# Kernel tuning notes

Hardware: AMD Instinct MI355X
Metric: run time of the kernel (lower is better)

Reference implementation:

```python
import jax, jax.numpy as jnp
import numpy as np

PH, PW = 7, 7
SPATIAL_SCALE = 1.0


def setup_inputs() -> dict:
    key = jax.random.key(0)
    kf, kb, kx, ky = jax.random.split(key, 4)
    B, C, H, W, R = 4, 256, 50, 50, 300
    feature_maps = jax.random.normal(kf, (B, C, H, W), dtype=jnp.float32)
    bidx = jax.random.randint(kb, (R,), 0, B).astype(jnp.float32)
    xs = jax.random.uniform(kx, (R, 2), minval=0.0, maxval=W - 1.0)
    ys = jax.random.uniform(ky, (R, 2), minval=0.0, maxval=H - 1.0)
    x_min = jnp.min(xs, axis=1)
    x_max = jnp.max(xs, axis=1)
    y_min = jnp.min(ys, axis=1)
    y_max = jnp.max(ys, axis=1)
    rois = jnp.stack([x_min, y_min, x_max, y_max, bidx], axis=1)  # [R,5]
    return {"feature_maps": feature_maps, "rois": rois}


def _roi_pool(feature_maps, rois):
    B, C, H, W = feature_maps.shape
    s = SPATIAL_SCALE
    r = rois * s                              # first scale application (as in source)
    batch_idx = r[:, 4].astype(jnp.int32)     # int() truncation of scaled batch index
    # second scale application + round + clamp, faithful to source's double-scaling
    x0 = jnp.clip(jnp.round(r[:, 0] * s), 0, W - 1).astype(jnp.int32)
    x1 = jnp.clip(jnp.round(r[:, 2] * s), 0, W - 1).astype(jnp.int32)
    y0 = jnp.clip(jnp.round(r[:, 1] * s), 0, H - 1).astype(jnp.int32)
    y1 = jnp.clip(jnp.round(r[:, 3] * s), 0, H - 1).astype(jnp.int32)
    x1 = jnp.maximum(x1, x0 + 1)
    y1 = jnp.maximum(y1, y0 + 1)
    roi_w = x1 - x0                           # >= 1, so every adaptive bin is nonempty
    roi_h = y1 - y0

    Kw = -(-W // PW)                          # max adaptive bin width  (ceil(W/PW))
    Kh = -(-H // PH)                          # max adaptive bin height (ceil(H/PH))

    # adaptive_max_pool2d bin edges: start = floor(i*size/out), end = ceil((i+1)*size/out)
    pw = jnp.arange(PW)
    wstart = x0[:, None] + (pw[None, :] * roi_w[:, None]) // PW                       # [R,PW]
    wend = x0[:, None] + ((pw[None, :] + 1) * roi_w[:, None] + PW - 1) // PW          # [R,PW]
    kw = jnp.arange(Kw)
    wpos = wstart[:, :, None] + kw[None, None, :]                                      # [R,PW,Kw]
    widx = jnp.clip(wpos, 0, W - 1)
    wvalid = wpos < wend[:, :, None]

    ph = jnp.arange(PH)
    hstart = y0[:, None] + (ph[None, :] * roi_h[:, None]) // PH
    hend = y0[:, None] + ((ph[None, :] + 1) * roi_h[:, None] + PH - 1) // PH
    kh = jnp.arange(Kh)
    hpos = hstart[:, :, None] + kh[None, None, :]                                      # [R,PH,Kh]
    hidx = jnp.clip(hpos, 0, H - 1)
    hvalid = hpos < hend[:, :, None]

    NEG = jnp.finfo(feature_maps.dtype).min
    fm = feature_maps[batch_idx]              # [R,C,H,W] per-ROI source map

    def gather_w(fm_r, widx_r):               # fm_r [C,H,W], widx_r [PW,Kw]
        return fm_r[:, :, widx_r]             # [C,H,PW,Kw]

    g = jax.vmap(gather_w)(fm, widx)          # [R,C,H,PW,Kw]
    A = jnp.max(jnp.where(wvalid[:, None, None, :, :], g, NEG), axis=-1)  # [R,C,H,PW]

    def gather_h(A_r, hidx_r):                # A_r [C,H,PW], hidx_r [PH,Kh]
        return A_r[:, hidx_r, :]              # [C,PH,Kh,PW]

    g2 = jax.vmap(gather_h)(A, hidx)          # [R,C,PH,Kh,PW]
    out = jnp.max(jnp.where(hvalid[:, None, :, :, None], g2, NEG), axis=3)  # [R,C,PH,PW]
    return out


def reference(feature_maps, rois):
    return _roi_pool(feature_maps, rois)
```

## Files before the change

kernel.cpp:

```cpp
#include <hip/hip_runtime.h>
#include <hip/hip_bf16.h>
#include <float.h>

#define B_  4
#define C_  256
#define H_  50
#define W_  50
#define R_  300
#define PH_ 7
#define PW_ 7
#define S_  (H_ * W_)
#define Q_  (PH_ * PW_)
#define SC_ (S_ * C_)
#define CQ_  64
#define NCQ  (C_ / CQ_)
#define NWG_POOL (R_ * NCQ)

__global__ __launch_bounds__(256) void transpose_tables(
    const float* __restrict__ fm,
    float* __restrict__ fmT,
    float* __restrict__ P2,
    float* __restrict__ P4)
{
    __shared__ float tile[64][69];

    const int b  = blockIdx.z;
    const int c0 = blockIdx.y * 64;
    const int s0 = blockIdx.x * 64;

    const int tx = threadIdx.x;
    const int ty = threadIdx.y;

    if (s0 + tx < S_) {
        #pragma unroll
        for (int j = 0; j < 16; ++j) {
            const int c = c0 + ty + j * 4;
            tile[ty + j * 4][tx] = fm[((size_t)b * C_ + c) * S_ + (s0 + tx)];
        }
    }
    if (tx < 4 && s0 + 64 + tx < S_) {
        #pragma unroll
        for (int j = 0; j < 16; ++j) {
            const int c = c0 + ty + j * 4;
            tile[ty + j * 4][64 + tx] = fm[((size_t)b * C_ + c) * S_ + (s0 + 64 + tx)];
        }
    }
    __syncthreads();

    #pragma unroll
    for (int j = 0; j < 16; ++j) {
        const int s = s0 + ty + j * 4;
        if (s < S_) {
            const int ls  = ty + j * 4;
            const int w   = s % W_;
            const int rem = W_ - 1 - w;
            const float v0 = tile[tx][ls];
            float p2 = (rem >= 1) ? fmaxf(v0, tile[tx][ls + 1]) : v0;
            float p4 = p2;
            if (rem >= 2) p4 = fmaxf(p4, tile[tx][ls + 2]);
            if (rem >= 3) p4 = fmaxf(p4, tile[tx][ls + 3]);

            const size_t o = ((size_t)b * S_ + s) * C_ + (c0 + tx);
            fmT[o] = v0;
            P2[o]  = p2;
            P4[o]  = p4;
        }
    }
}

__device__ __forceinline__ void roi_decode(const float* __restrict__ rois, int r,
                                           int& b, int& x0, int& y0,
                                           int& roi_w, int& roi_h)
{
    const float* rp = rois + r * 5;
    b = (int)rp[4];
    x0      = (int)rintf(rp[0]);
    y0      = (int)rintf(rp[1]);
    int x1  = (int)rintf(rp[2]);
    int y1  = (int)rintf(rp[3]);
    x0 = min(max(x0, 0), W_ - 1);
    x1 = min(max(x1, 0), W_ - 1);
    y0 = min(max(y0, 0), H_ - 1);
    y1 = min(max(y1, 0), H_ - 1);
    x1 = max(x1, x0 + 1);
    y1 = max(y1, y0 + 1);
    roi_w = x1 - x0;
    roi_h = y1 - y0;
}

template<int WH>
__device__ __forceinline__ void pool_bins(
    const float* __restrict__ fmT, const float* __restrict__ P2,
    const float* __restrict__ P4, float* __restrict__ buf,
    int wv, int lane, int imgC,
    int x0, int y0, int roi_w, int roi_h)
{
    const int start = wv * 12 + (wv ? 1 : 0);
    const int qlast = wv * 12 + 12;

    #pragma unroll 2
    for (int k = 0; k < 13; ++k) {
        int q = start + k;
        q = (q > qlast) ? qlast : q;
        const int ph = q / PW_;
        const int pw = q - ph * PW_;
        const int ws = x0 + (pw * roi_w) / PW_;
        const int we = x0 + ((pw + 1) * roi_w + PW_ - 1) / PW_;
        const int hs = y0 + (ph * roi_h) / PH_;
        const int he = y0 + ((ph + 1) * roi_h + PH_ - 1) / PH_;
        const int ww = we - ws;

        const int sp = (ww >= 4) ? 4 : ((ww >= 2) ? 2 : 1);
        const float* tb = (ww >= 4) ? P4 : ((ww >= 2) ? P2 : fmT);
        const int colB = we - sp;

        float va[WH], vb[WH];
        #pragma unroll
        for (int kh = 0; kh < WH; ++kh) {
            int row = hs + kh;
            row = (row > he - 1) ? (he - 1) : row;
            const int ro = imgC + row * (W_ * C_);
            va[kh] = tb[ro + ws * C_];
            vb[kh] = tb[ro + colB * C_];
        }
        float m = -FLT_MAX;
        #pragma unroll
        for (int kh = 0; kh < WH; ++kh)
            m = fmaxf(m, fmaxf(va[kh], vb[kh]));

        buf[q * 65 + lane] = m;
    }
}

__global__ __launch_bounds__(256) void roi_pool_tables(
    const float* __restrict__ fmT,
    const float* __restrict__ P2,
    const float* __restrict__ P4,
    const float* __restrict__ rois,
    float* __restrict__ out)
{
    __shared__ float buf[Q_ * 65];

    const int bid = blockIdx.x;
    const int swz = (bid & 7) * (NWG_POOL / 8) + (bid >> 3);
    const int r   = swz >> 2;
    const int c0  = (swz & (NCQ - 1)) * CQ_;

    const int t    = threadIdx.x;
    const int wv   = t >> 6;
    const int lane = t & 63;

    int b, x0, y0, roi_w, roi_h;
    roi_decode(rois, r, b, x0, y0, roi_w, roi_h);

    int whmax = 1;
    #pragma unroll
    for (int i = 0; i < PH_; ++i) {
        const int hs = (i * roi_h) / PH_;
        const int he = ((i + 1) * roi_h + PH_ - 1) / PH_;
        whmax = max(whmax, he - hs);
    }

    const int imgC = b * SC_ + c0 + lane;

    switch (whmax) {
        case 1: pool_bins<1>(fmT, P2, P4, buf, wv, lane, imgC, x0, y0, roi_w, roi_h); break;
        case 2: pool_bins<2>(fmT, P2, P4, buf, wv, lane, imgC, x0, y0, roi_w, roi_h); break;
        case 3: pool_bins<3>(fmT, P2, P4, buf, wv, lane, imgC, x0, y0, roi_w, roi_h); break;
        case 4: pool_bins<4>(fmT, P2, P4, buf, wv, lane, imgC, x0, y0, roi_w, roi_h); break;
        case 5: pool_bins<5>(fmT, P2, P4, buf, wv, lane, imgC, x0, y0, roi_w, roi_h); break;
        case 6: pool_bins<6>(fmT, P2, P4, buf, wv, lane, imgC, x0, y0, roi_w, roi_h); break;
        case 7: pool_bins<7>(fmT, P2, P4, buf, wv, lane, imgC, x0, y0, roi_w, roi_h); break;
        default: pool_bins<8>(fmT, P2, P4, buf, wv, lane, imgC, x0, y0, roi_w, roi_h); break;
    }
    __syncthreads();

    float* outp = out + ((size_t)r * C_ + c0) * Q_;
    #pragma unroll
    for (int k = 0; k < 13; ++k) {
        const int e = k * 256 + t;
        if (e < CQ_ * Q_) {
            const int cl = e / Q_;
            const int q  = e - cl * Q_;
            outp[e] = buf[q * 65 + cl];
        }
    }
}

__global__ __launch_bounds__(256) void roi_pool_naive(
    const float* __restrict__ fm,
    const float* __restrict__ rois,
    float* __restrict__ out)
{
    const int total = R_ * C_ * Q_;
    int t = blockIdx.x * blockDim.x + threadIdx.x;
    if (t >= total) return;
    int q   = t % Q_;
    int tmp = t / Q_;
    int pw  = q % PW_;
    int ph  = q / PW_;
    int c   = tmp % C_;
    int r   = tmp / C_;

    int b, x0, y0, roi_w, roi_h;
    roi_decode(rois, r, b, x0, y0, roi_w, roi_h);

    const int ws = x0 + (pw * roi_w) / PW_;
    const int we = x0 + ((pw + 1) * roi_w + PW_ - 1) / PW_;
    const int hs = y0 + (ph * roi_h) / PH_;
    const int he = y0 + ((ph + 1) * roi_h + PH_ - 1) / PH_;

    const float* p = fm + ((size_t)(b * C_ + c)) * S_;
    float m = -FLT_MAX;
    for (int h = hs; h < he; ++h)
        for (int w = ws; w < we; ++w)
            m = fmaxf(m, p[h * W_ + w]);
    out[t] = m;
}

extern "C" void kernel_launch(void* const* d_in, const int* in_sizes, int n_in,
                              void* d_out, int out_size, void* d_ws, size_t ws_size,
                              hipStream_t stream)
{
    const float* fm   = (const float*)d_in[0];
    const float* rois = (const float*)d_in[1];
    float* out        = (float*)d_out;

    const size_t ARR  = (size_t)B_ * SC_;
    const size_t NEED = 3 * ARR * sizeof(float);

    if (ws_size >= NEED) {
        float* fmT = (float*)d_ws;
        float* P2  = fmT + ARR;
        float* P4  = P2 + ARR;
        {
            dim3 grid((S_ + 63) / 64, C_ / 64, B_);
            dim3 block(64, 4, 1);
            transpose_tables<<<grid, block, 0, stream>>>(fm, fmT, P2, P4);
        }
        roi_pool_tables<<<NWG_POOL, 256, 0, stream>>>(fmT, P2, P4, rois, out);
    } else {
        const int total = R_ * C_ * Q_;
        roi_pool_naive<<<(total + 255) / 256, 256, 0, stream>>>(fm, rois, out);
    }
}
```

Measured before the change: 33.70 us.

## Drop P2 table, use three-column fmT reads, and sort ROIs for locality

```diff
diff --git a/kernel.cpp b/kernel.cpp
--- a/kernel.cpp
+++ b/kernel.cpp
@@ -12,6 +12,7 @@
 #define S_  (H_ * W_)
 #define Q_  (PH_ * PW_)
 #define SC_ (S_ * C_)
+#define ARRN (B_ * SC_)
 #define CQ_  64
 #define NCQ  (C_ / CQ_)
 #define NWG_POOL (R_ * NCQ)
@@ -19,10 +20,35 @@
 __global__ __launch_bounds__(256) void transpose_tables(
     const float* __restrict__ fm,
     float* __restrict__ fmT,
-    float* __restrict__ P2,
-    float* __restrict__ P4)
+    float* __restrict__ P4,
+    const float* __restrict__ rois,
+    int* __restrict__ perm)
 {
     __shared__ float tile[64][69];
+    __shared__ int   skey[R_];
+
+    if (blockIdx.x == 40) {
+        if (blockIdx.y != 0 || blockIdx.z != 0) return;
+        const int t = threadIdx.y * 64 + threadIdx.x;
+        for (int i = t; i < R_; i += 256) {
+            const float* rp = rois + i * 5;
+            int b  = (int)rp[4];
+            int x0 = (int)rintf(rp[0]); x0 = min(max(x0, 0), W_ - 1);
+            int y0 = (int)rintf(rp[1]); y0 = min(max(y0, 0), H_ - 1);
+            skey[i] = (b << 8) | ((y0 >> 3) << 4) | (x0 >> 3);
+        }
+        __syncthreads();
+        for (int i = t; i < R_; i += 256) {
+            const int k = skey[i];
+            int rank = 0;
+            for (int j = 0; j < R_; ++j) {
+                const int kj = skey[j];
+                rank += (kj < k) || (kj == k && j < i);
+            }
+            perm[rank] = i;
+        }
+        return;
+    }
 
     const int b  = blockIdx.z;
     const int c0 = blockIdx.y * 64;
@@ -55,14 +81,13 @@
             const int w   = s % W_;
             const int rem = W_ - 1 - w;
             const float v0 = tile[tx][ls];
-            float p2 = (rem >= 1) ? fmaxf(v0, tile[tx][ls + 1]) : v0;
-            float p4 = p2;
+            float p4 = v0;
+            if (rem >= 1) p4 = fmaxf(p4, tile[tx][ls + 1]);
             if (rem >= 2) p4 = fmaxf(p4, tile[tx][ls + 2]);
             if (rem >= 3) p4 = fmaxf(p4, tile[tx][ls + 3]);
 
             const size_t o = ((size_t)b * S_ + s) * C_ + (c0 + tx);
             fmT[o] = v0;
-            P2[o]  = p2;
             P4[o]  = p4;
         }
     }
@@ -90,8 +115,8 @@
 
 template<int WH>
 __device__ __forceinline__ void pool_bins(
-    const float* __restrict__ fmT, const float* __restrict__ P2,
-    const float* __restrict__ P4, float* __restrict__ buf,
+    const float* __restrict__ fmT, const float* __restrict__ P4,
+    float* __restrict__ buf,
     int wv, int lane, int imgC,
     int x0, int y0, int roi_w, int roi_h)
 {
@@ -110,41 +135,57 @@
         const int he = y0 + ((ph + 1) * roi_h + PH_ - 1) / PH_;
         const int ww = we - ws;
 
-        const int sp = (ww >= 4) ? 4 : ((ww >= 2) ? 2 : 1);
-        const float* tb = (ww >= 4) ? P4 : ((ww >= 2) ? P2 : fmT);
-        const int colB = we - sp;
-
-        float va[WH], vb[WH];
-        #pragma unroll
-        for (int kh = 0; kh < WH; ++kh) {
-            int row = hs + kh;
-            row = (row > he - 1) ? (he - 1) : row;
-            const int ro = imgC + row * (W_ * C_);
-            va[kh] = tb[ro + ws * C_];
-            vb[kh] = tb[ro + colB * C_];
-        }
         float m = -FLT_MAX;
-        #pragma unroll
-        for (int kh = 0; kh < WH; ++kh)
-            m = fmaxf(m, fmaxf(va[kh], vb[kh]));
-
+        if (ww >= 4) {
+            const int cA = ws * C_, cB = (we - 4) * C_;
+            float va[WH], vb[WH];
+            #pragma unroll
+            for (int kh = 0; kh < WH; ++kh) {
+                int row = hs + kh;
+                row = (row > he - 1) ? (he - 1) : row;
+                const int ro = imgC + row * (W_ * C_);
+                va[kh] = P4[ro + cA];
+                vb[kh] = P4[ro + cB];
+            }
+            #pragma unroll
+            for (int kh = 0; kh < WH; ++kh)
+                m = fmaxf(m, fmaxf(va[kh], vb[kh]));
+        } else {
+            const int cA = ws * C_;
+            const int cB = min(ws + 1, we - 1) * C_;
+            const int cC = (we - 1) * C_;
+            float va[WH], vb[WH], vc[WH];
+            #pragma unroll
+            for (int kh = 0; kh < WH; ++kh) {
+                int row = hs + kh;
+                row = (row > he - 1) ? (he - 1) : row;
+                const int ro = imgC + row * (W_ * C_);
+                va[kh] = fmT[ro + cA];
+                vb[kh] = fmT[ro + cB];
+                vc[kh] = fmT[ro + cC];
+            }
+            #pragma unroll
+            for (int kh = 0; kh < WH; ++kh)
+                m = fmaxf(m, fmaxf(va[kh], fmaxf(vb[kh], vc[kh])));
+        }
         buf[q * 65 + lane] = m;
     }
 }
 
 __global__ __launch_bounds__(256) void roi_pool_tables(
     const float* __restrict__ fmT,
-    const float* __restrict__ P2,
     const float* __restrict__ P4,
     const float* __restrict__ rois,
+    const int* __restrict__ perm,
     float* __restrict__ out)
 {
     __shared__ float buf[Q_ * 65];
 
     const int bid = blockIdx.x;
     const int swz = (bid & 7) * (NWG_POOL / 8) + (bid >> 3);
-    const int r   = swz >> 2;
+    const int rid = swz >> 2;
     const int c0  = (swz & (NCQ - 1)) * CQ_;
+    const int r   = perm[rid];
 
     const int t    = threadIdx.x;
     const int wv   = t >> 6;
@@ -164,14 +205,14 @@
     const int imgC = b * SC_ + c0 + lane;
 
     switch (whmax) {
-        case 1: pool_bins<1>(fmT, P2, P4, buf, wv, lane, imgC, x0, y0, roi_w, roi_h); break;
-        case 2: pool_bins<2>(fmT, P2, P4, buf, wv, lane, imgC, x0, y0, roi_w, roi_h); break;
-        case 3: pool_bins<3>(fmT, P2, P4, buf, wv, lane, imgC, x0, y0, roi_w, roi_h); break;
-        case 4: pool_bins<4>(fmT, P2, P4, buf, wv, lane, imgC, x0, y0, roi_w, roi_h); break;
-        case 5: pool_bins<5>(fmT, P2, P4, buf, wv, lane, imgC, x0, y0, roi_w, roi_h); break;
-        case 6: pool_bins<6>(fmT, P2, P4, buf, wv, lane, imgC, x0, y0, roi_w, roi_h); break;
-        case 7: pool_bins<7>(fmT, P2, P4, buf, wv, lane, imgC, x0, y0, roi_w, roi_h); break;
-        default: pool_bins<8>(fmT, P2, P4, buf, wv, lane, imgC, x0, y0, roi_w, roi_h); break;
+        case 1: pool_bins<1>(fmT, P4, buf, wv, lane, imgC, x0, y0, roi_w, roi_h); break;
+        case 2: pool_bins<2>(fmT, P4, buf, wv, lane, imgC, x0, y0, roi_w, roi_h); break;
+        case 3: pool_bins<3>(fmT, P4, buf, wv, lane, imgC, x0, y0, roi_w, roi_h); break;
+        case 4: pool_bins<4>(fmT, P4, buf, wv, lane, imgC, x0, y0, roi_w, roi_h); break;
+        case 5: pool_bins<5>(fmT, P4, buf, wv, lane, imgC, x0, y0, roi_w, roi_h); break;
+        case 6: pool_bins<6>(fmT, P4, buf, wv, lane, imgC, x0, y0, roi_w, roi_h); break;
+        case 7: pool_bins<7>(fmT, P4, buf, wv, lane, imgC, x0, y0, roi_w, roi_h); break;
+        default: pool_bins<8>(fmT, P4, buf, wv, lane, imgC, x0, y0, roi_w, roi_h); break;
     }
     __syncthreads();
 
@@ -226,19 +267,18 @@
     const float* rois = (const float*)d_in[1];
     float* out        = (float*)d_out;
 
-    const size_t ARR  = (size_t)B_ * SC_;
-    const size_t NEED = 3 * ARR * sizeof(float);
+    const size_t NEED = 2 * (size_t)ARRN * sizeof(float) + 4096;
 
     if (ws_size >= NEED) {
         float* fmT = (float*)d_ws;
-        float* P2  = fmT + ARR;
-        float* P4  = P2 + ARR;
+        float* P4  = fmT + ARRN;
+        int*   perm = (int*)(P4 + ARRN);
         {
-            dim3 grid((S_ + 63) / 64, C_ / 64, B_);
+            dim3 grid(41, C_ / 64, B_);
             dim3 block(64, 4, 1);
-            transpose_tables<<<grid, block, 0, stream>>>(fm, fmT, P2, P4);
-        }
-        roi_pool_tables<<<NWG_POOL, 256, 0, stream>>>(fmT, P2, P4, rois, out);
+            transpose_tables<<<grid, block, 0, stream>>>(fm, fmT, P4, rois, perm);
+        }
+        roi_pool_tables<<<NWG_POOL, 256, 0, stream>>>(fmT, P4, rois, perm, out);
     } else {
         const int total = R_ * C_ * Q_;
         roi_pool_naive<<<(total + 255) / 256, 256, 0, stream>>>(fm, rois, out);
```

After: 43.35 us. +28.7%, slower.

## Sort ROIs by batch and spatial tile to improve cache locality in pooling

Applied to the files above, without the earlier changes.

```diff
diff --git a/kernel.cpp b/kernel.cpp
--- a/kernel.cpp
+++ b/kernel.cpp
@@ -12,6 +12,7 @@
 #define S_  (H_ * W_)
 #define Q_  (PH_ * PW_)
 #define SC_ (S_ * C_)
+#define ARRN (B_ * SC_)
 #define CQ_  64
 #define NCQ  (C_ / CQ_)
 #define NWG_POOL (R_ * NCQ)
@@ -20,9 +21,35 @@
     const float* __restrict__ fm,
     float* __restrict__ fmT,
     float* __restrict__ P2,
-    float* __restrict__ P4)
+    float* __restrict__ P4,
+    const float* __restrict__ rois,
+    int* __restrict__ perm)
 {
     __shared__ float tile[64][69];
+    __shared__ int   skey[R_];
+
+    if (blockIdx.x == 40) {
+        if (blockIdx.y != 0 || blockIdx.z != 0) return;
+        const int t = threadIdx.y * 64 + threadIdx.x;
+        for (int i = t; i < R_; i += 256) {
+            const float* rp = rois + i * 5;
+            int b  = (int)rp[4];
+            int x0 = (int)rintf(rp[0]); x0 = min(max(x0, 0), W_ - 1);
+            int y0 = (int)rintf(rp[1]); y0 = min(max(y0, 0), H_ - 1);
+            skey[i] = (b << 8) | ((y0 >> 3) << 4) | (x0 >> 3);
+        }
+        __syncthreads();
+        for (int i = t; i < R_; i += 256) {
+            const int k = skey[i];
+            int rank = 0;
+            for (int j = 0; j < R_; ++j) {
+                const int kj = skey[j];
+                rank += (kj < k) || (kj == k && j < i);
+            }
+            perm[rank] = i;
+        }
+        return;
+    }
 
     const int b  = blockIdx.z;
     const int c0 = blockIdx.y * 64;
@@ -137,14 +164,16 @@
     const float* __restrict__ P2,
     const float* __restrict__ P4,
     const float* __restrict__ rois,
+    const int* __restrict__ perm,
     float* __restrict__ out)
 {
     __shared__ float buf[Q_ * 65];
 
     const int bid = blockIdx.x;
     const int swz = (bid & 7) * (NWG_POOL / 8) + (bid >> 3);
-    const int r   = swz >> 2;
+    const int rid = swz >> 2;
     const int c0  = (swz & (NCQ - 1)) * CQ_;
+    const int r   = perm[rid];
 
     const int t    = threadIdx.x;
     const int wv   = t >> 6;
@@ -226,19 +255,19 @@
     const float* rois = (const float*)d_in[1];
     float* out        = (float*)d_out;
 
-    const size_t ARR  = (size_t)B_ * SC_;
-    const size_t NEED = 3 * ARR * sizeof(float);
+    const size_t NEED = 3 * (size_t)ARRN * sizeof(float) + 4096;
 
     if (ws_size >= NEED) {
-        float* fmT = (float*)d_ws;
-        float* P2  = fmT + ARR;
-        float* P4  = P2 + ARR;
+        float* fmT  = (float*)d_ws;
+        float* P2   = fmT + ARRN;
+        float* P4   = P2 + ARRN;
+        int*   perm = (int*)(P4 + ARRN);
         {
-            dim3 grid((S_ + 63) / 64, C_ / 64, B_);
+            dim3 grid(41, C_ / 64, B_);
             dim3 block(64, 4, 1);
-            transpose_tables<<<grid, block, 0, stream>>>(fm, fmT, P2, P4);
-        }
-        roi_pool_tables<<<NWG_POOL, 256, 0, stream>>>(fmT, P2, P4, rois, out);
+            transpose_tables<<<grid, block, 0, stream>>>(fm, fmT, P2, P4, rois, perm);
+        }
+        roi_pool_tables<<<NWG_POOL, 256, 0, stream>>>(fmT, P2, P4, rois, perm, out);
     } else {
         const int total = R_ * C_ * Q_;
         roi_pool_naive<<<(total + 255) / 256, 256, 0, stream>>>(fm, rois, out);
```

Measured after the change: 42.19 us. 25.2% more time.

## Split ROI pooling into 32-channel blocks with half-wave column split

Applied to the files above, without the earlier changes.

```diff
diff --git a/kernel.cpp b/kernel.cpp
--- a/kernel.cpp
+++ b/kernel.cpp
@@ -12,9 +12,10 @@
 #define S_  (H_ * W_)
 #define Q_  (PH_ * PW_)
 #define SC_ (S_ * C_)
-#define CQ_  64
-#define NCQ  (C_ / CQ_)
-#define NWG_POOL (R_ * NCQ)
+#define ARRN (B_ * SC_)
+#define CE_  32
+#define NCE  (C_ / CE_)
+#define NWG_POOL (R_ * NCE)
 
 __global__ __launch_bounds__(256) void transpose_tables(
     const float* __restrict__ fm,
@@ -89,62 +90,62 @@
 }
 
 template<int WH>
-__device__ __forceinline__ void pool_bins(
+__device__ __forceinline__ void pool_bins_e(
     const float* __restrict__ fmT, const float* __restrict__ P2,
     const float* __restrict__ P4, float* __restrict__ buf,
-    int wv, int lane, int imgC,
+    int wv, int lane, int imgCE,
     int x0, int y0, int roi_w, int roi_h)
 {
-    const int start = wv * 12 + (wv ? 1 : 0);
-    const int qlast = wv * 12 + 12;
+    const int c    = lane & 31;
+    const int half = lane >> 5;
 
     #pragma unroll 2
-    for (int k = 0; k < 13; ++k) {
-        int q = start + k;
-        q = (q > qlast) ? qlast : q;
-        const int ph = q / PW_;
-        const int pw = q - ph * PW_;
-        const int ws = x0 + (pw * roi_w) / PW_;
-        const int we = x0 + ((pw + 1) * roi_w + PW_ - 1) / PW_;
-        const int hs = y0 + (ph * roi_h) / PH_;
-        const int he = y0 + ((ph + 1) * roi_h + PH_ - 1) / PH_;
-        const int ww = we - ws;
-
-        const int sp = (ww >= 4) ? 4 : ((ww >= 2) ? 2 : 1);
-        const float* tb = (ww >= 4) ? P4 : ((ww >= 2) ? P2 : fmT);
-        const int colB = we - sp;
-
-        float va[WH], vb[WH];
-        #pragma unroll
-        for (int kh = 0; kh < WH; ++kh) {
-            int row = hs + kh;
-            row = (row > he - 1) ? (he - 1) : row;
-            const int ro = imgC + row * (W_ * C_);
-            va[kh] = tb[ro + ws * C_];
-            vb[kh] = tb[ro + colB * C_];
-        }
-        float m = -FLT_MAX;
-        #pragma unroll
-        for (int kh = 0; kh < WH; ++kh)
-            m = fmaxf(m, fmaxf(va[kh], vb[kh]));
-
-        buf[q * 65 + lane] = m;
-    }
-}
-
-__global__ __launch_bounds__(256) void roi_pool_tables(
+    for (int k = 0; k < 25; ++k) {
+        const int q = wv + 2 * k;
+        if (q < Q_) {
+            const int ph = q / PW_;
+            const int pw = q - ph * PW_;
+            const int ws = x0 + (pw * roi_w) / PW_;
+            const int we = x0 + ((pw + 1) * roi_w + PW_ - 1) / PW_;
+            const int hs = y0 + (ph * roi_h) / PH_;
+            const int he = y0 + ((ph + 1) * roi_h + PH_ - 1) / PH_;
+            const int ww = we - ws;
+
+            const int sp = (ww >= 4) ? 4 : ((ww >= 2) ? 2 : 1);
+            const float* tb = (ww >= 4) ? P4 : ((ww >= 2) ? P2 : fmT);
+            const int col = (half ? (we - sp) : ws) * C_;
+
+            float va[WH];
+            #pragma unroll
+            for (int kh = 0; kh < WH; ++kh) {
+                int row = hs + kh;
+                row = (row > he - 1) ? (he - 1) : row;
+                va[kh] = tb[imgCE + row * (W_ * C_) + col];
+            }
+            float m = -FLT_MAX;
+            #pragma unroll
+            for (int kh = 0; kh < WH; ++kh)
+                m = fmaxf(m, va[kh]);
+
+            m = fmaxf(m, __shfl_xor(m, 32));
+            if (half == 0)
+                buf[q * 33 + c] = m;
+        }
+    }
+}
+
+__global__ __launch_bounds__(128) void roi_pool_tables(
     const float* __restrict__ fmT,
     const float* __restrict__ P2,
     const float* __restrict__ P4,
     const float* __restrict__ rois,
     float* __restrict__ out)
 {
-    __shared__ float buf[Q_ * 65];
+    __shared__ float buf[Q_ * 33];
 
     const int bid = blockIdx.x;
-    const int swz = (bid & 7) * (NWG_POOL / 8) + (bid >> 3);
-    const int r   = swz >> 2;
-    const int c0  = (swz & (NCQ - 1)) * CQ_;
+    const int e   = bid & 7;
+    const int r   = bid >> 3;
 
     const int t    = threadIdx.x;
     const int wv   = t >> 6;
@@ -161,28 +162,28 @@
         whmax = max(whmax, he - hs);
     }
 
-    const int imgC = b * SC_ + c0 + lane;
+    const int imgCE = b * SC_ + e * CE_ + (lane & 31);
 
     switch (whmax) {
-        case 1: pool_bins<1>(fmT, P2, P4, buf, wv, lane, imgC, x0, y0, roi_w, roi_h); break;
-        case 2: pool_bins<2>(fmT, P2, P4, buf, wv, lane, imgC, x0, y0, roi_w, roi_h); break;
-        case 3: pool_bins<3>(fmT, P2, P4, buf, wv, lane, imgC, x0, y0, roi_w, roi_h); break;
-        case 4: pool_bins<4>(fmT, P2, P4, buf, wv, lane, imgC, x0, y0, roi_w, roi_h); break;
-        case 5: pool_bins<5>(fmT, P2, P4, buf, wv, lane, imgC, x0, y0, roi_w, roi_h); break;
-        case 6: pool_bins<6>(fmT, P2, P4, buf, wv, lane, imgC, x0, y0, roi_w, roi_h); break;
-        case 7: pool_bins<7>(fmT, P2, P4, buf, wv, lane, imgC, x0, y0, roi_w, roi_h); break;
-        default: pool_bins<8>(fmT, P2, P4, buf, wv, lane, imgC, x0, y0, roi_w, roi_h); break;
+        case 1: pool_bins_e<1>(fmT, P2, P4, buf, wv, lane, imgCE, x0, y0, roi_w, roi_h); break;
+        case 2: pool_bins_e<2>(fmT, P2, P4, buf, wv, lane, imgCE, x0, y0, roi_w, roi_h); break;
+        case 3: pool_bins_e<3>(fmT, P2, P4, buf, wv, lane, imgCE, x0, y0, roi_w, roi_h); break;
+        case 4: pool_bins_e<4>(fmT, P2, P4, buf, wv, lane, imgCE, x0, y0, roi_w, roi_h); break;
+        case 5: pool_bins_e<5>(fmT, P2, P4, buf, wv, lane, imgCE, x0, y0, roi_w, roi_h); break;
+        case 6: pool_bins_e<6>(fmT, P2, P4, buf, wv, lane, imgCE, x0, y0, roi_w, roi_h); break;
+        case 7: pool_bins_e<7>(fmT, P2, P4, buf, wv, lane, imgCE, x0, y0, roi_w, roi_h); break;
+        default: pool_bins_e<8>(fmT, P2, P4, buf, wv, lane, imgCE, x0, y0, roi_w, roi_h); break;
     }
     __syncthreads();
 
-    float* outp = out + ((size_t)r * C_ + c0) * Q_;
+    float* outp = out + ((size_t)r * C_ + e * CE_) * Q_;
     #pragma unroll
     for (int k = 0; k < 13; ++k) {
-        const int e = k * 256 + t;
-        if (e < CQ_ * Q_) {
-            const int cl = e / Q_;
-            const int q  = e - cl * Q_;
-            outp[e] = buf[q * 65 + cl];
+        const int idx = k * 128 + t;
+        if (idx < CE_ * Q_) {
+            const int cl = idx / Q_;
+            const int q  = idx - cl * Q_;
+            outp[idx] = buf[q * 33 + cl];
         }
     }
 }
@@ -226,19 +227,18 @@
     const float* rois = (const float*)d_in[1];
     float* out        = (float*)d_out;
 
-    const size_t ARR  = (size_t)B_ * SC_;
-    const size_t NEED = 3 * ARR * sizeof(float);
+    const size_t NEED = 3 * (size_t)ARRN * sizeof(float);
 
     if (ws_size >= NEED) {
         float* fmT = (float*)d_ws;
-        float* P2  = fmT + ARR;
-        float* P4  = P2 + ARR;
+        float* P2  = fmT + ARRN;
+        float* P4  = P2 + ARRN;
         {
-            dim3 grid((S_ + 63) / 64, C_ / 64, B_);
+            dim3 grid(40, C_ / 64, B_);
             dim3 block(64, 4, 1);
             transpose_tables<<<grid, block, 0, stream>>>(fm, fmT, P2, P4);
         }
-        roi_pool_tables<<<NWG_POOL, 256, 0, stream>>>(fmT, P2, P4, rois, out);
+        roi_pool_tables<<<NWG_POOL, 128, 0, stream>>>(fmT, P2, P4, rois, out);
     } else {
         const int total = R_ * C_ * Q_;
         roi_pool_naive<<<(total + 255) / 256, 256, 0, stream>>>(fm, rois, out);
```

New measurement: 41.10 us. 22.0% more time.
